# Kernel optimization log

Hardware: AMD Instinct MI355X
Metric: run time of the kernel (lower is better)

Reference implementation:

```python
import jax, jax.numpy as jnp
import numpy as np

TEMPERATURE = 0.6
TOP_K = 50
TOP_P = 0.9
REP_PENALTY = 1.2
BATCH, VOCAB, HIST = 256, 128000, 200


def setup_inputs() -> dict:
    key = jax.random.key(0)
    k1, k2 = jax.random.split(key)
    logits = jax.random.normal(k1, (BATCH, VOCAB), dtype=jnp.float32)
    prev_tokens = jax.random.randint(k2, (BATCH, HIST), 0, VOCAB)
    return {"logits": logits, "prev_tokens": prev_tokens}


def reference(logits, prev_tokens):
    B = logits.shape[0]
    rows = jnp.arange(B)[:, None]  # [B,1] row index for scatter

    # --- repetition penalty: mult if <0 else div, on previously seen tokens ---
    vals = jnp.take_along_axis(logits, prev_tokens, axis=1)  # [B,H]
    penalized = jnp.where(vals < 0, vals * REP_PENALTY, vals / REP_PENALTY)
    logits = logits.at[rows, prev_tokens].set(penalized)

    # --- temperature ---
    logits = logits / TEMPERATURE

    # --- top-k filter: mask everything below the k-th largest logit ---
    kth = jax.lax.top_k(logits, TOP_K)[0][:, -1:]  # [B,1]
    logits = jnp.where(logits < kth, -jnp.inf, logits)

    # --- top-p (nucleus) filter: sort desc, cumsum probs, keep prefix <= p ---
    order = jnp.argsort(-logits, axis=-1)                      # [B,V] desc order
    sorted_logits = jnp.take_along_axis(logits, order, axis=-1)
    cum_probs = jnp.cumsum(jax.nn.softmax(sorted_logits, axis=-1), axis=-1)
    remove_sorted = cum_probs > TOP_P
    # shift right so the first token exceeding p is kept (HF semantics)
    remove_sorted = jnp.concatenate(
        [jnp.zeros_like(remove_sorted[:, :1]), remove_sorted[:, :-1]], axis=-1)
    # scatter mask back to vocab order
    remove = jnp.zeros_like(remove_sorted).at[rows, order].set(remove_sorted)
    logits = jnp.where(remove, -jnp.inf, logits)

    # --- distribution parameter of Multinomial(total_count=compare_sample) ---
    probs = jax.nn.softmax(logits, axis=-1)
    return probs
```

## Files before the change

### kernel.cpp

```cpp
#include <hip/hip_runtime.h>
#include <stdint.h>

#define BATCH    256
#define VOCAB    128000
#define HIST     200
#define TOPK     50
#define BITWORDS (VOCAB / 32)

#define SLICES   8
#define NT1      256
#define NT2      256
#define LCAP     1024
#define TRAW     3.0f

#define CAP      2048
#define NTHREADS 1024

typedef float f32x4_t __attribute__((ext_vector_type(4)));

__device__ __forceinline__ unsigned fkey_of(float f) {
  unsigned u = __float_as_uint(f);
  return (u & 0x80000000u) ? ~u : (u | 0x80000000u);
}
__device__ __forceinline__ float f_of_key(unsigned k) {
  unsigned u = (k & 0x80000000u) ? (k & 0x7FFFFFFFu) : ~k;
  return __uint_as_float(u);
}

__global__ __launch_bounds__(NT1) void stream_collect_kernel(
    const float* __restrict__ logits, float* __restrict__ out,
    int* __restrict__ cnt_g, uint2* __restrict__ cand_g)
{
  const int bid = blockIdx.x;
  const int b = bid >> 3;
  const int s = bid & (SLICES - 1);
  const float4* row4  = (const float4*)(logits + (size_t)b * VOCAB);
  float4*       orow4 = (float4*)(out + (size_t)b * VOCAB);
  const int per = (VOCAB / 4) / SLICES;
  const int lo = s * per, hi = lo + per;
  int*   cnt  = cnt_g + b;
  uint2* cand = cand_g + (size_t)b * LCAP;

  const f32x4_t z4 = (f32x4_t)0.f;
  for (int i = lo + threadIdx.x; i < hi; i += NT1) {
    float4 v = row4[i];
    __builtin_nontemporal_store(z4, (f32x4_t*)&orow4[i]);
    unsigned v0 = 4u * (unsigned)i;
    if (v.x > TRAW) { int p = atomicAdd(cnt, 1); if (p < LCAP) cand[p] = make_uint2(__float_as_uint(v.x), v0 + 0u); }
    if (v.y > TRAW) { int p = atomicAdd(cnt, 1); if (p < LCAP) cand[p] = make_uint2(__float_as_uint(v.y), v0 + 1u); }
    if (v.z > TRAW) { int p = atomicAdd(cnt, 1); if (p < LCAP) cand[p] = make_uint2(__float_as_uint(v.z), v0 + 2u); }
    if (v.w > TRAW) { int p = atomicAdd(cnt, 1); if (p < LCAP) cand[p] = make_uint2(__float_as_uint(v.w), v0 + 3u); }
  }
}

__global__ __launch_bounds__(NT2) void select_kernel(
    const float* __restrict__ logits, const int* __restrict__ prev,
    float* __restrict__ out, const int* __restrict__ cnt_g,
    const uint2* __restrict__ cand_g)
{
  __shared__ unsigned bitmask[BITWORDS];
  __shared__ unsigned long long keys[LCAP];
  __shared__ float evals[LCAP];
  __shared__ int s_cnt, s_good, s_m, s_j;
  __shared__ float s_maxx, s_Z2;

  const int b   = blockIdx.x;
  const int tid = threadIdx.x;
  const float* row  = logits + (size_t)b * VOCAB;
  float*       orow = out    + (size_t)b * VOCAB;

  for (int i = tid; i < BITWORDS; i += NT2) bitmask[i] = 0u;
  if (tid == 0) s_good = 0;
  __syncthreads();
  for (int i = tid; i < HIST; i += NT2) {
    int t = prev[b * HIST + i];
    atomicOr(&bitmask[t >> 5], 1u << (t & 31));
  }
  __syncthreads();

  int cnt = cnt_g[b];
  int mn = cnt < LCAP ? cnt : LCAP;
  const uint2* cand = cand_g + (size_t)b * LCAP;
  for (int i = tid; i < mn; i += NT2) {
    uint2 c = cand[i];
    float v = __uint_as_float(c.x);
    unsigned idx = c.y;
    float y = v;
    if ((bitmask[idx >> 5] >> (idx & 31)) & 1u)
      y = (v < 0.0f) ? v * 1.2f : v / 1.2f;
    float x = y / 0.6f;
    keys[i] = ((unsigned long long)fkey_of(x) << 32) |
              (unsigned)(~idx);
    if (y > TRAW) atomicAdd(&s_good, 1);
  }
  __syncthreads();

  if (cnt > LCAP || s_good < TOPK) {
    float T = TRAW;
    float Tlo = 0.f, Thi = 0.f;
    bool hasLo = false, hasHi = false;
    const float4* row4 = (const float4*)row;
    const int N4 = VOCAB / 4;
    for (int attempt = 0; attempt < 40; ++attempt) {
      __syncthreads();
      if (tid == 0) s_cnt = 0;
      __syncthreads();
      for (int i = tid; i < N4; i += NT2) {
        float4 v4 = row4[i];
        int v0 = i * 4;
        unsigned w  = bitmask[v0 >> 5];
        unsigned sh = v0 & 31;
        float vv[4] = {v4.x, v4.y, v4.z, v4.w};
        #pragma unroll
        for (int l = 0; l < 4; ++l) {
          float v = vv[l];
          float y = v;
          if ((w >> (sh + l)) & 1u)
            y = (v < 0.0f) ? v * 1.2f : v / 1.2f;
          if (y > T) {
            int pos = atomicAdd(&s_cnt, 1);
            if (pos < LCAP) {
              unsigned k = fkey_of(y / 0.6f);
              keys[pos] = ((unsigned long long)k << 32) |
                          (unsigned)(~(unsigned)(v0 + l));
            }
          }
        }
      }
      __syncthreads();
      cnt = s_cnt;
      if (cnt >= TOPK && cnt <= LCAP) break;
      if (cnt < TOPK) { Thi = T; hasHi = true; T = hasLo ? 0.5f * (T + Tlo) : T - 1.0f; }
      else            { Tlo = T; hasLo = true; T = hasHi ? 0.5f * (T + Thi) : T + 1.0f; }
    }
    if (cnt > LCAP) cnt = LCAP;
  }

  int n = 64;
  while (n < cnt) n <<= 1;
  for (int i = cnt + tid; i < n; i += NT2) keys[i] = 0ull;
  __syncthreads();
  for (int k = 2; k <= n; k <<= 1) {
    for (int j = k >> 1; j > 0; j >>= 1) {
      for (int i = tid; i < n; i += NT2) {
        int l = i ^ j;
        if (l > i) {
          unsigned long long a = keys[i], c = keys[l];
          bool up = (i & k) == 0;
          if (up ? (a < c) : (a > c)) { keys[i] = c; keys[l] = a; }
        }
      }
      __syncthreads();
    }
  }

  if (tid == 0) {
    int kk = (cnt < TOPK) ? cnt : TOPK;
    unsigned kth = (unsigned)(keys[kk - 1] >> 32);
    int m = kk;
    while (m < cnt && (unsigned)(keys[m] >> 32) == kth) m++;
    s_m = m;
    s_maxx = f_of_key((unsigned)(keys[0] >> 32));
  }
  __syncthreads();
  int m = s_m;
  float maxx = s_maxx;
  for (int i = tid; i < m; i += NT2)
    evals[i] = expf(f_of_key((unsigned)(keys[i] >> 32)) - maxx);
  __syncthreads();

  if (tid == 0) {
    float Z = 0.f;
    for (int i = 0; i < m; ++i) Z += evals[i];
    float cum = 0.f;
    int j = 0;
    for (int i = 0; i < m; ++i) {
      if (i > 0 && cum > 0.9f) break;
      cum += evals[i] / Z;
      j = i + 1;
    }
    float Z2 = 0.f;
    for (int i = 0; i < j; ++i) Z2 += evals[i];
    s_j = j; s_Z2 = Z2;
  }
  __syncthreads();

  int j = s_j;
  float Z2 = s_Z2;
  for (int i = tid; i < j; i += NT2) {
    int idx = (int)(~(unsigned)(keys[i] & 0xFFFFFFFFull));
    orow[idx] = evals[i] / Z2;
  }
}

__global__ __launch_bounds__(NTHREADS) void sample_head_kernel(
    const float* __restrict__ logits, const int* __restrict__ prev,
    float* __restrict__ out)
{
  __shared__ unsigned bitmask[BITWORDS];
  __shared__ unsigned long long keys[CAP];
  __shared__ float evals[CAP];
  __shared__ int s_count;
  __shared__ int s_m, s_j;
  __shared__ float s_maxx, s_Z2;

  const int b   = blockIdx.x;
  const int tid = threadIdx.x;
  const float* row  = logits + (size_t)b * VOCAB;
  float*       orow = out    + (size_t)b * VOCAB;

  for (int i = tid; i < BITWORDS; i += NTHREADS) bitmask[i] = 0u;
  __syncthreads();
  for (int i = tid; i < HIST; i += NTHREADS) {
    int t = prev[b * HIST + i];
    atomicOr(&bitmask[t >> 5], 1u << (t & 31));
  }
  __syncthreads();

  float T = 3.0f;
  float Tlo = 0.f, Thi = 0.f;
  bool hasLo = false, hasHi = false;
  int cnt = 0;

  const float4* row4  = (const float4*)row;
  float4*       orow4 = (float4*)orow;
  const int N4 = VOCAB / 4;

  for (int attempt = 0; attempt < 40; ++attempt) {
    __syncthreads();
    if (tid == 0) s_count = 0;
    __syncthreads();

    for (int i = tid; i < N4; i += NTHREADS) {
      float4 v4 = row4[i];
      if (attempt == 0) orow4[i] = make_float4(0.f, 0.f, 0.f, 0.f);
      int v0 = i * 4;
      unsigned w  = bitmask[v0 >> 5];
      unsigned sh = v0 & 31;
      float vv[4] = {v4.x, v4.y, v4.z, v4.w};
      #pragma unroll
      for (int l = 0; l < 4; ++l) {
        float v = vv[l];
        float y = v;
        if ((w >> (sh + l)) & 1u)
          y = (v < 0.0f) ? v * 1.2f : v / 1.2f;
        if (y > T) {
          float x = y / 0.6f;
          int pos = atomicAdd(&s_count, 1);
          if (pos < CAP) {
            unsigned k = fkey_of(x);
            keys[pos] = ((unsigned long long)k << 32) |
                        (unsigned)(~(unsigned)(v0 + l));
          }
        }
      }
    }
    __syncthreads();
    cnt = s_count;
    if (cnt >= TOPK && cnt <= CAP) break;
    if (cnt < TOPK) { Thi = T; hasHi = true; T = hasLo ? 0.5f * (T + Tlo) : T - 1.0f; }
    else            { Tlo = T; hasLo = true; T = hasHi ? 0.5f * (T + Thi) : T + 1.0f; }
  }
  if (cnt > CAP) cnt = CAP;

  int n = 64;
  while (n < cnt) n <<= 1;
  for (int i = cnt + tid; i < n; i += NTHREADS) keys[i] = 0ull;
  __syncthreads();
  for (int k = 2; k <= n; k <<= 1) {
    for (int j = k >> 1; j > 0; j >>= 1) {
      for (int i = tid; i < n; i += NTHREADS) {
        int l = i ^ j;
        if (l > i) {
          unsigned long long a = keys[i], c = keys[l];
          bool up = (i & k) == 0;
          if (up ? (a < c) : (a > c)) { keys[i] = c; keys[l] = a; }
        }
      }
      __syncthreads();
    }
  }

  if (tid == 0) {
    int kk = (cnt < TOPK) ? cnt : TOPK;
    unsigned kth = (unsigned)(keys[kk - 1] >> 32);
    int m = kk;
    while (m < cnt && (unsigned)(keys[m] >> 32) == kth) m++;
    s_m = m;
    s_maxx = f_of_key((unsigned)(keys[0] >> 32));
  }
  __syncthreads();
  int m = s_m;
  float maxx = s_maxx;
  for (int i = tid; i < m; i += NTHREADS)
    evals[i] = expf(f_of_key((unsigned)(keys[i] >> 32)) - maxx);
  __syncthreads();

  if (tid == 0) {
    float Z = 0.f;
    for (int i = 0; i < m; ++i) Z += evals[i];
    float cum = 0.f;
    int j = 0;
    for (int i = 0; i < m; ++i) {
      if (i > 0 && cum > 0.9f) break;
      cum += evals[i] / Z;
      j = i + 1;
    }
    float Z2 = 0.f;
    for (int i = 0; i < j; ++i) Z2 += evals[i];
    s_j = j; s_Z2 = Z2;
  }
  __syncthreads();

  int j = s_j;
  float Z2 = s_Z2;
  for (int i = tid; i < j; i += NTHREADS) {
    int idx = (int)(~(unsigned)(keys[i] & 0xFFFFFFFFull));
    orow[idx] = evals[i] / Z2;
  }
}

extern "C" void kernel_launch(void* const* d_in, const int* in_sizes, int n_in,
                              void* d_out, int out_size, void* d_ws, size_t ws_size,
                              hipStream_t stream) {
  const float* logits = (const float*)d_in[0];
  const int*   prev   = (const int*)d_in[1];
  float*       out    = (float*)d_out;

  const size_t cnt_bytes  = (size_t)BATCH * sizeof(int);
  const size_t cand_off   = 1024;
  const size_t need       = cand_off + (size_t)BATCH * LCAP * sizeof(uint2);

  if (d_ws != nullptr && ws_size >= need) {
    int*   cnt_g  = (int*)d_ws;
    uint2* cand_g = (uint2*)((char*)d_ws + cand_off);
    hipMemsetAsync(d_ws, 0, cnt_bytes, stream);
    hipLaunchKernelGGL(stream_collect_kernel, dim3(BATCH * SLICES), dim3(NT1),
                       0, stream, logits, out, cnt_g, cand_g);
    hipLaunchKernelGGL(select_kernel, dim3(BATCH), dim3(NT2),
                       0, stream, logits, prev, out, cnt_g, cand_g);
  } else {
    hipLaunchKernelGGL(sample_head_kernel, dim3(BATCH), dim3(NTHREADS),
                       0, stream, logits, prev, out);
  }
}
```

Baseline: 258.1 us.

## Unroll stream loads by four, replace bitonic sort with rank sort, widen select block

The streaming kernel now issues four float4 loads and zero stores per iteration, giving more memory-level parallelism before the threshold checks. In the select kernel the multi-pass bitonic sort with many barriers becomes a single-pass rank (counting) sort into a second shared buffer. The select block grows from 256 to 512 threads. Rank sort costs O(cnt^2) comparisons per row and adds 8KB of shared memory, which could lower occupancy, but keys are unique (index in low bits), so ranks are unique.

```diff
diff --git a/kernel.cpp b/kernel.cpp
--- a/kernel.cpp
+++ b/kernel.cpp
@@ -9,7 +9,7 @@
 
 #define SLICES   8
 #define NT1      256
-#define NT2      256
+#define NT2      512
 #define LCAP     1024
 #define TRAW     3.0f
 
@@ -25,6 +25,15 @@
 __device__ __forceinline__ float f_of_key(unsigned k) {
   unsigned u = (k & 0x80000000u) ? (k & 0x7FFFFFFFu) : ~k;
   return __uint_as_float(u);
+}
+
+__device__ __forceinline__ void push4(float4 v, unsigned v0,
+                                      int* __restrict__ cnt,
+                                      uint2* __restrict__ cand) {
+  if (v.x > TRAW) { int p = atomicAdd(cnt, 1); if (p < LCAP) cand[p] = make_uint2(__float_as_uint(v.x), v0 + 0u); }
+  if (v.y > TRAW) { int p = atomicAdd(cnt, 1); if (p < LCAP) cand[p] = make_uint2(__float_as_uint(v.y), v0 + 1u); }
+  if (v.z > TRAW) { int p = atomicAdd(cnt, 1); if (p < LCAP) cand[p] = make_uint2(__float_as_uint(v.z), v0 + 2u); }
+  if (v.w > TRAW) { int p = atomicAdd(cnt, 1); if (p < LCAP) cand[p] = make_uint2(__float_as_uint(v.w), v0 + 3u); }
 }
 
 __global__ __launch_bounds__(NT1) void stream_collect_kernel(
@@ -42,14 +51,26 @@
   uint2* cand = cand_g + (size_t)b * LCAP;
 
   const f32x4_t z4 = (f32x4_t)0.f;
-  for (int i = lo + threadIdx.x; i < hi; i += NT1) {
-    float4 v = row4[i];
+  int i = lo + (int)threadIdx.x;
+
+  for (; i + 3 * NT1 < hi; i += 4 * NT1) {
+    float4 a = row4[i];
+    float4 b4 = row4[i + NT1];
+    float4 c = row4[i + 2 * NT1];
+    float4 d = row4[i + 3 * NT1];
     __builtin_nontemporal_store(z4, (f32x4_t*)&orow4[i]);
-    unsigned v0 = 4u * (unsigned)i;
-    if (v.x > TRAW) { int p = atomicAdd(cnt, 1); if (p < LCAP) cand[p] = make_uint2(__float_as_uint(v.x), v0 + 0u); }
-    if (v.y > TRAW) { int p = atomicAdd(cnt, 1); if (p < LCAP) cand[p] = make_uint2(__float_as_uint(v.y), v0 + 1u); }
-    if (v.z > TRAW) { int p = atomicAdd(cnt, 1); if (p < LCAP) cand[p] = make_uint2(__float_as_uint(v.z), v0 + 2u); }
-    if (v.w > TRAW) { int p = atomicAdd(cnt, 1); if (p < LCAP) cand[p] = make_uint2(__float_as_uint(v.w), v0 + 3u); }
+    __builtin_nontemporal_store(z4, (f32x4_t*)&orow4[i + NT1]);
+    __builtin_nontemporal_store(z4, (f32x4_t*)&orow4[i + 2 * NT1]);
+    __builtin_nontemporal_store(z4, (f32x4_t*)&orow4[i + 3 * NT1]);
+    push4(a, 4u * (unsigned)i, cnt, cand);
+    push4(b4, 4u * (unsigned)(i + NT1), cnt, cand);
+    push4(c, 4u * (unsigned)(i + 2 * NT1), cnt, cand);
+    push4(d, 4u * (unsigned)(i + 3 * NT1), cnt, cand);
+  }
+  for (; i < hi; i += NT1) {
+    float4 a = row4[i];
+    __builtin_nontemporal_store(z4, (f32x4_t*)&orow4[i]);
+    push4(a, 4u * (unsigned)i, cnt, cand);
   }
 }
 
@@ -60,6 +81,7 @@
 {
   __shared__ unsigned bitmask[BITWORDS];
   __shared__ unsigned long long keys[LCAP];
+  __shared__ unsigned long long skeys[LCAP];
   __shared__ float evals[LCAP];
   __shared__ int s_cnt, s_good, s_m, s_j;
   __shared__ float s_maxx, s_Z2;
@@ -136,37 +158,27 @@
     if (cnt > LCAP) cnt = LCAP;
   }
 
-  int n = 64;
-  while (n < cnt) n <<= 1;
-  for (int i = cnt + tid; i < n; i += NT2) keys[i] = 0ull;
-  __syncthreads();
-  for (int k = 2; k <= n; k <<= 1) {
-    for (int j = k >> 1; j > 0; j >>= 1) {
-      for (int i = tid; i < n; i += NT2) {
-        int l = i ^ j;
-        if (l > i) {
-          unsigned long long a = keys[i], c = keys[l];
-          bool up = (i & k) == 0;
-          if (up ? (a < c) : (a > c)) { keys[i] = c; keys[l] = a; }
-        }
-      }
-      __syncthreads();
-    }
-  }
+  for (int i = tid; i < cnt; i += NT2) {
+    unsigned long long a = keys[i];
+    int r = 0;
+    for (int j = 0; j < cnt; ++j) r += (keys[j] > a);
+    skeys[r] = a;
+  }
+  __syncthreads();
 
   if (tid == 0) {
     int kk = (cnt < TOPK) ? cnt : TOPK;
-    unsigned kth = (unsigned)(keys[kk - 1] >> 32);
+    unsigned kth = (unsigned)(skeys[kk - 1] >> 32);
     int m = kk;
-    while (m < cnt && (unsigned)(keys[m] >> 32) == kth) m++;
+    while (m < cnt && (unsigned)(skeys[m] >> 32) == kth) m++;
     s_m = m;
-    s_maxx = f_of_key((unsigned)(keys[0] >> 32));
+    s_maxx = f_of_key((unsigned)(skeys[0] >> 32));
   }
   __syncthreads();
   int m = s_m;
   float maxx = s_maxx;
   for (int i = tid; i < m; i += NT2)
-    evals[i] = expf(f_of_key((unsigned)(keys[i] >> 32)) - maxx);
+    evals[i] = expf(f_of_key((unsigned)(skeys[i] >> 32)) - maxx);
   __syncthreads();
 
   if (tid == 0) {
@@ -188,7 +200,7 @@
   int j = s_j;
   float Z2 = s_Z2;
   for (int i = tid; i < j; i += NT2) {
-    int idx = (int)(~(unsigned)(keys[i] & 0xFFFFFFFFull));
+    int idx = (int)(~(unsigned)(skeys[i] & 0xFFFFFFFFull));
     orow[idx] = evals[i] / Z2;
   }
 }
```

After: 279.5 us. 8.3% more time.
